# Kernel optimization log

Measured on AMD Instinct MI355X. Metric: run time of the kernel, lower is better.

Reference implementation:

```python
import jax, jax.numpy as jnp
import numpy as np

B, L, D, H = 8, 1024, 512, 8
DH = D // H  # 64
EPS = 1e-5


def setup_inputs() -> dict:
    key = jax.random.key(0)
    ks = jax.random.split(key, 9)
    query = jax.random.normal(ks[0], (B, L, D), dtype=jnp.float32)
    key_t = jax.random.normal(ks[1], (B, L, D), dtype=jnp.float32)
    value = jax.random.normal(ks[2], (B, L, D), dtype=jnp.float32)
    attn_mask = jax.random.bernoulli(ks[3], 0.1, (B, L, L))
    softmax_mask = jax.random.bernoulli(ks[4], 0.1, (B, L, L))
    s = 1.0 / np.sqrt(D)
    Wq = jax.random.uniform(ks[5], (D, D), jnp.float32, -s, s)
    Wk = jax.random.uniform(ks[6], (D, D), jnp.float32, -s, s)
    Wv = jax.random.uniform(ks[7], (D, D), jnp.float32, -s, s)
    Wo = jax.random.uniform(ks[8], (D, D), jnp.float32, -s, s)
    return {"query": query, "key": key_t, "value": value,
            "attn_mask": attn_mask, "softmax_mask": softmax_mask,
            "Wq": Wq, "Wk": Wk, "Wv": Wv, "Wo": Wo}


def _split_heads(x):
    # [B, L, D] -> [B, H, L, DH]
    b, l, _ = x.shape
    return x.reshape(b, l, H, DH).transpose(0, 2, 1, 3)


def reference(query, key, value, attn_mask, softmax_mask, Wq, Wk, Wv, Wo):
    residual = query
    q = _split_heads(query @ Wq.T)   # [B,H,L,DH]
    k = _split_heads(key @ Wk.T)
    v = _split_heads(value @ Wv.T)
    scale = DH ** (-0.5)
    scores = jnp.einsum("bhqd,bhkd->bhqk", q, k) * scale
    scores = jnp.where(attn_mask[:, None], -jnp.inf, scores)
    attention = jax.nn.softmax(scores, axis=-1)
    attention = jnp.where(softmax_mask[:, None], 0.0, attention)
    # dropout p = 0.0 -> identity
    context = jnp.einsum("bhqk,bhkd->bhqd", attention, v)
    context = context.transpose(0, 2, 1, 3).reshape(query.shape[0], -1, D)
    output = context @ Wo.T
    x = residual + output
    mean = jnp.mean(x, axis=-1, keepdims=True)
    var = jnp.var(x, axis=-1, keepdims=True)
    out = (x - mean) * jax.lax.rsqrt(var + EPS)  # LayerNorm, no affine
    return out, attention
```

## Files before the change

### kernel.cpp

```cpp
#include <hip/hip_runtime.h>

#define BB 8
#define LL 1024
#define DD 512
#define HH 8

typedef __attribute__((ext_vector_type(8))) short bf16x8;
typedef __attribute__((ext_vector_type(4))) float f32x4;

__device__ __forceinline__ unsigned short f2bf(float f) {
    union { float f; unsigned u; } c; c.f = f;
    unsigned u = c.u + 0x7fffu + ((c.u >> 16) & 1u);
    return (unsigned short)(u >> 16);
}

__global__ __launch_bounds__(256) void castw_kernel(
    const float* wq, const float* wk, const float* wv, const float* wo,
    unsigned short* wqb, unsigned short* wkb, unsigned short* wvb, unsigned short* wob)
{
    const float* src; unsigned short* dst;
    switch (blockIdx.y) {
        case 0:  src = wq; dst = wqb; break;
        case 1:  src = wk; dst = wkb; break;
        case 2:  src = wv; dst = wvb; break;
        default: src = wo; dst = wob; break;
    }
    const int g = (blockIdx.x * 256 + threadIdx.x) * 8;
    const float4 a = *reinterpret_cast<const float4*>(src + g);
    const float4 b = *reinterpret_cast<const float4*>(src + g + 4);
    uint4 o;
    o.x = (unsigned)f2bf(a.x) | ((unsigned)f2bf(a.y) << 16);
    o.y = (unsigned)f2bf(a.z) | ((unsigned)f2bf(a.w) << 16);
    o.z = (unsigned)f2bf(b.x) | ((unsigned)f2bf(b.y) << 16);
    o.w = (unsigned)f2bf(b.z) | ((unsigned)f2bf(b.w) << 16);
    *reinterpret_cast<uint4*>(dst + g) = o;
}

__global__ __launch_bounds__(256) void maskpack_kernel(
    const int* __restrict__ am, const int* __restrict__ sm,
    unsigned* __restrict__ ab, unsigned* __restrict__ sb)
{
    const int* src = blockIdx.y ? sm : am;
    unsigned* dst  = blockIdx.y ? sb : ab;
    const int l = threadIdx.x & 63;
    for (int g = blockIdx.x * 256 + threadIdx.x; g < 8388608; g += gridDim.x * 256) {
        unsigned long long bm = __ballot(src[g] != 0);
        if (l == 0)  dst[g >> 5] = (unsigned)bm;
        if (l == 32) dst[g >> 5] = (unsigned)(bm >> 32);
    }
}

template<bool OUTBF, bool AF32>
__device__ __forceinline__ void gemm_mfma_body(
    const void* __restrict__ Av, const unsigned short* __restrict__ W,
    void* __restrict__ Yv)
{
    __shared__ unsigned short As[128 * 40];
    __shared__ unsigned short Bs[128 * 40];
    const int t = threadIdx.x, w = t >> 6, lane = t & 63;
    const int ln15 = lane & 15, quad = lane >> 4;
    const int wm = w & 1, wn = w >> 1;
    const int m0 = blockIdx.y * 128, n0 = blockIdx.x * 128;
    f32x4 acc[4][4];
    #pragma unroll
    for (int i = 0; i < 4; i++)
        #pragma unroll
        for (int j = 0; j < 4; j++) acc[i][j] = (f32x4){0.f, 0.f, 0.f, 0.f};

    for (int k0 = 0; k0 < 512; k0 += 32) {
        uint4 ga[2], gb[2];
        #pragma unroll
        for (int i = 0; i < 2; i++) {
            const int u = t + i * 256, row = u >> 2, ch = (u & 3) * 8;
            if (AF32) {
                const float* Af = (const float*)Av;
                const float4 fa = *reinterpret_cast<const float4*>(&Af[(size_t)(m0 + row) * 512 + k0 + ch]);
                const float4 fb = *reinterpret_cast<const float4*>(&Af[(size_t)(m0 + row) * 512 + k0 + ch + 4]);
                ga[i].x = (unsigned)f2bf(fa.x) | ((unsigned)f2bf(fa.y) << 16);
                ga[i].y = (unsigned)f2bf(fa.z) | ((unsigned)f2bf(fa.w) << 16);
                ga[i].z = (unsigned)f2bf(fb.x) | ((unsigned)f2bf(fb.y) << 16);
                ga[i].w = (unsigned)f2bf(fb.z) | ((unsigned)f2bf(fb.w) << 16);
            } else {
                ga[i] = *reinterpret_cast<const uint4*>(
                    &((const unsigned short*)Av)[(size_t)(m0 + row) * 512 + k0 + ch]);
            }
            gb[i] = *reinterpret_cast<const uint4*>(&W[(size_t)(n0 + row) * 512 + k0 + ch]);
        }
        if (k0) __syncthreads();
        #pragma unroll
        for (int i = 0; i < 2; i++) {
            const int u = t + i * 256, row = u >> 2, ch = (u & 3) * 8;
            *reinterpret_cast<uint4*>(&As[row * 40 + ch]) = ga[i];
            *reinterpret_cast<uint4*>(&Bs[row * 40 + ch]) = gb[i];
        }
        __syncthreads();
        bf16x8 af[4], bf_[4];
        #pragma unroll
        for (int s = 0; s < 4; s++) {
            af[s]  = *reinterpret_cast<const bf16x8*>(&As[(wm * 64 + s * 16 + ln15) * 40 + quad * 8]);
            bf_[s] = *reinterpret_cast<const bf16x8*>(&Bs[(wn * 64 + s * 16 + ln15) * 40 + quad * 8]);
        }
        #pragma unroll
        for (int sm_ = 0; sm_ < 4; sm_++)
            #pragma unroll
            for (int sn_ = 0; sn_ < 4; sn_++)
                acc[sm_][sn_] = __builtin_amdgcn_mfma_f32_16x16x32_bf16(
                    af[sm_], bf_[sn_], acc[sm_][sn_], 0, 0, 0);
    }
    #pragma unroll
    for (int sm_ = 0; sm_ < 4; sm_++)
        #pragma unroll
        for (int sn_ = 0; sn_ < 4; sn_++)
            #pragma unroll
            for (int r = 0; r < 4; r++) {
                const int row = m0 + wm * 64 + sm_ * 16 + quad * 4 + r;
                const int col = n0 + wn * 64 + sn_ * 16 + ln15;
                if (OUTBF)
                    ((unsigned short*)Yv)[(size_t)row * 512 + col] = f2bf(acc[sm_][sn_][r]);
                else
                    ((float*)Yv)[(size_t)row * 512 + col] = acc[sm_][sn_][r];
            }
}

__global__ __launch_bounds__(256) void gemm3_kernel(
    const float* a0, const float* a1, const float* a2,
    const unsigned short* w0, const unsigned short* w1, const unsigned short* w2,
    unsigned short* y0, unsigned short* y1, unsigned short* y2)
{
    const float* A; const unsigned short* W; unsigned short* Y;
    if (blockIdx.z == 0)      { A = a0; W = w0; Y = y0; }
    else if (blockIdx.z == 1) { A = a1; W = w1; Y = y1; }
    else                      { A = a2; W = w2; Y = y2; }
    gemm_mfma_body<true, true>(A, W, Y);
}

__global__ __launch_bounds__(256) void gemm1_kernel(
    const unsigned short* A, const unsigned short* W, float* Y)
{
    gemm_mfma_body<false, false>(A, W, Y);
}

__global__ __launch_bounds__(256) void vtrans_kernel(
    const unsigned short* __restrict__ Vb, unsigned short* __restrict__ Vt)
{
    __shared__ unsigned short tile[64 * 72];
    const int t = threadIdx.x;
    const int tt = blockIdx.x, h = blockIdx.y, b = blockIdx.z;
    #pragma unroll
    for (int i = 0; i < 2; i++) {
        const int u = t + i * 256, row = u >> 3, ch = (u & 7) * 8;
        *reinterpret_cast<uint4*>(&tile[row * 72 + ch]) =
            *reinterpret_cast<const uint4*>(&Vb[(size_t)(b * 1024 + tt * 64 + row) * 512 + h * 64 + ch]);
    }
    __syncthreads();
    #pragma unroll
    for (int i = 0; i < 2; i++) {
        const int u = t + i * 256, dh = u >> 3, ch = (u & 7) * 8;
        unsigned short r8[8];
        #pragma unroll
        for (int e = 0; e < 8; e++) r8[e] = tile[(ch + e) * 72 + dh];
        uint4 o;
        o.x = (unsigned)r8[0] | ((unsigned)r8[1] << 16);
        o.y = (unsigned)r8[2] | ((unsigned)r8[3] << 16);
        o.z = (unsigned)r8[4] | ((unsigned)r8[5] << 16);
        o.w = (unsigned)r8[6] | ((unsigned)r8[7] << 16);
        *reinterpret_cast<uint4*>(&Vt[(size_t)((b * 8 + h) * 64 + dh) * 1024 + tt * 64 + ch]) = o;
    }
}

__global__ __launch_bounds__(256) void fattn_kernel(
    const unsigned short* __restrict__ Qb, const unsigned short* __restrict__ Kb,
    const unsigned short* __restrict__ Vt,
    const unsigned* __restrict__ ab, const unsigned* __restrict__ sb,
    float* __restrict__ attn, unsigned short* __restrict__ CTX)
{
    __shared__ __align__(16) unsigned short Ks[64 * 72];
    __shared__ __align__(16) unsigned short Vs[64 * 72];
    __shared__ __align__(16) unsigned short Pt[4][16 * 72];
    const int t = threadIdx.x, w = t >> 6, lane = t & 63;
    const int ln15 = lane & 15, quad = lane >> 4;
    const int id = blockIdx.x;
    const int b = id & 7, slot = id >> 3;
    const int qt = slot & 15, h = slot >> 4;
    const int bh = b * 8 + h;
    const int qbase = qt * 64 + w * 16;

    const int srow = t >> 2, sch = (t & 3) * 16;
    const size_t kg = ((size_t)(b * 1024 + srow)) * 512 + h * 64 + sch;
    const size_t vg = ((size_t)(bh * 64 + srow)) * 1024 + sch;
    unsigned short* ksw = &Ks[srow * 72 + sch];
    unsigned short* vsw = &Vs[srow * 72 + sch];

    const size_t qoff = ((size_t)(b * 1024) + qbase + ln15) * 512 + h * 64 + quad * 8;
    const bf16x8 aq0 = *reinterpret_cast<const bf16x8*>(Qb + qoff);
    const bf16x8 aq1 = *reinterpret_cast<const bf16x8*>(Qb + qoff + 32);

    int mrow[4];
    #pragma unroll
    for (int r = 0; r < 4; r++)
        mrow[r] = (b * 1024 + qbase + quad * 4 + r) * 32;

    uint4 kr0 = *reinterpret_cast<const uint4*>(Kb + kg);
    uint4 kr1 = *reinterpret_cast<const uint4*>(Kb + kg + 8);
    *reinterpret_cast<uint4*>(ksw)     = kr0;
    *reinterpret_cast<uint4*>(ksw + 8) = kr1;
    __syncthreads();

    float l[4];
    #pragma unroll
    for (int r = 0; r < 4; r++) l[r] = 0.f;

    for (int kt = 0; kt < 16; kt++) {
        if (kt < 15) {
            kr0 = *reinterpret_cast<const uint4*>(Kb + kg + (size_t)(kt + 1) * 32768);
            kr1 = *reinterpret_cast<const uint4*>(Kb + kg + (size_t)(kt + 1) * 32768 + 8);
        }
        f32x4 acc[4];
        #pragma unroll
        for (int sub = 0; sub < 4; sub++) {
            const bf16x8 bk0 = *reinterpret_cast<const bf16x8*>(&Ks[(sub * 16 + ln15) * 72 + quad * 8]);
            const bf16x8 bk1 = *reinterpret_cast<const bf16x8*>(&Ks[(sub * 16 + ln15) * 72 + quad * 8 + 32]);
            f32x4 c = __builtin_amdgcn_mfma_f32_16x16x32_bf16(aq0, bk0, (f32x4){0.f,0.f,0.f,0.f}, 0, 0, 0);
            acc[sub] = __builtin_amdgcn_mfma_f32_16x16x32_bf16(aq1, bk1, c, 0, 0, 0);
        }
        #pragma unroll
        for (int r = 0; r < 4; r++) {
            const unsigned w0 = ab[mrow[r] + kt * 2], w1 = ab[mrow[r] + kt * 2 + 1];
            #pragma unroll
            for (int sub = 0; sub < 4; sub++) {
                const int cb = sub * 16 + ln15;
                const unsigned msk = ((cb & 32 ? w1 : w0) >> (cb & 31)) & 1u;
                const float e = __expf(acc[sub][r] * 0.125f);
                l[r] += msk ? 0.f : e;
            }
        }
        __syncthreads();
        if (kt < 15) {
            *reinterpret_cast<uint4*>(ksw)     = kr0;
            *reinterpret_cast<uint4*>(ksw + 8) = kr1;
        }
        __syncthreads();
    }
    float invl[4];
    #pragma unroll
    for (int r = 0; r < 4; r++) {
        #pragma unroll
        for (int off = 1; off < 16; off <<= 1) l[r] += __shfl_xor(l[r], off);
        invl[r] = 1.f / l[r];
    }

    kr0 = *reinterpret_cast<const uint4*>(Kb + kg);
    kr1 = *reinterpret_cast<const uint4*>(Kb + kg + 8);
    uint4 vr0 = *reinterpret_cast<const uint4*>(Vt + vg);
    uint4 vr1 = *reinterpret_cast<const uint4*>(Vt + vg + 8);
    __syncthreads();
    *reinterpret_cast<uint4*>(ksw)     = kr0;
    *reinterpret_cast<uint4*>(ksw + 8) = kr1;
    *reinterpret_cast<uint4*>(vsw)     = vr0;
    *reinterpret_cast<uint4*>(vsw + 8) = vr1;
    __syncthreads();

    f32x4 o[4];
    #pragma unroll
    for (int sn = 0; sn < 4; sn++) o[sn] = (f32x4){0.f, 0.f, 0.f, 0.f};
    unsigned short* Pw = Pt[w];

    for (int kt = 0; kt < 16; kt++) {
        if (kt < 15) {
            kr0 = *reinterpret_cast<const uint4*>(Kb + kg + (size_t)(kt + 1) * 32768);
            kr1 = *reinterpret_cast<const uint4*>(Kb + kg + (size_t)(kt + 1) * 32768 + 8);
            vr0 = *reinterpret_cast<const uint4*>(Vt + vg + (size_t)(kt + 1) * 64);
            vr1 = *reinterpret_cast<const uint4*>(Vt + vg + (size_t)(kt + 1) * 64 + 8);
        }
        f32x4 acc[4];
        #pragma unroll
        for (int sub = 0; sub < 4; sub++) {
            const bf16x8 bk0 = *reinterpret_cast<const bf16x8*>(&Ks[(sub * 16 + ln15) * 72 + quad * 8]);
            const bf16x8 bk1 = *reinterpret_cast<const bf16x8*>(&Ks[(sub * 16 + ln15) * 72 + quad * 8 + 32]);
            f32x4 c = __builtin_amdgcn_mfma_f32_16x16x32_bf16(aq0, bk0, (f32x4){0.f,0.f,0.f,0.f}, 0, 0, 0);
            acc[sub] = __builtin_amdgcn_mfma_f32_16x16x32_bf16(aq1, bk1, c, 0, 0, 0);
        }
        #pragma unroll
        for (int r = 0; r < 4; r++) {
            const unsigned a0 = ab[mrow[r] + kt * 2], a1 = ab[mrow[r] + kt * 2 + 1];
            const unsigned s0 = sb[mrow[r] + kt * 2], s1 = sb[mrow[r] + kt * 2 + 1];
            #pragma unroll
            for (int sub = 0; sub < 4; sub++) {
                const int cb = sub * 16 + ln15;
                const unsigned amsk = ((cb & 32 ? a1 : a0) >> (cb & 31)) & 1u;
                const unsigned smsk = ((cb & 32 ? s1 : s0) >> (cb & 31)) & 1u;
                float a = __expf(acc[sub][r] * 0.125f) * invl[r];
                a = amsk ? 0.f : a;
                a = smsk ? 0.f : a;
                attn[((size_t)bh * 1024 + qbase + quad * 4 + r) * 1024 + kt * 64 + cb] = a;
                Pw[(quad * 4 + r) * 72 + cb] = f2bf(a);
            }
        }
        const bf16x8 pa0 = *reinterpret_cast<const bf16x8*>(&Pw[ln15 * 72 + quad * 8]);
        const bf16x8 pa1 = *reinterpret_cast<const bf16x8*>(&Pw[ln15 * 72 + 32 + quad * 8]);
        #pragma unroll
        for (int sn = 0; sn < 4; sn++) {
            const bf16x8 vb0 = *reinterpret_cast<const bf16x8*>(&Vs[(sn * 16 + ln15) * 72 + quad * 8]);
            const bf16x8 vb1 = *reinterpret_cast<const bf16x8*>(&Vs[(sn * 16 + ln15) * 72 + quad * 8 + 32]);
            o[sn] = __builtin_amdgcn_mfma_f32_16x16x32_bf16(pa0, vb0, o[sn], 0, 0, 0);
            o[sn] = __builtin_amdgcn_mfma_f32_16x16x32_bf16(pa1, vb1, o[sn], 0, 0, 0);
        }
        __syncthreads();
        if (kt < 15) {
            *reinterpret_cast<uint4*>(ksw)     = kr0;
            *reinterpret_cast<uint4*>(ksw + 8) = kr1;
            *reinterpret_cast<uint4*>(vsw)     = vr0;
            *reinterpret_cast<uint4*>(vsw + 8) = vr1;
        }
        __syncthreads();
    }
    #pragma unroll
    for (int sn = 0; sn < 4; sn++)
        #pragma unroll
        for (int r = 0; r < 4; r++)
            CTX[((size_t)(b * 1024) + qbase + quad * 4 + r) * 512 + h * 64 + sn * 16 + ln15] =
                f2bf(o[sn][r]);
}

__global__ __launch_bounds__(256) void ln_kernel(
    const float* __restrict__ X, const float* __restrict__ R,
    float* __restrict__ out)
{
    __shared__ float rs[4], rq[4];
    const int r = blockIdx.x, t = threadIdx.x;
    const float2 xv = *reinterpret_cast<const float2*>(&X[(size_t)r * 512 + 2 * t]);
    const float2 rv = *reinterpret_cast<const float2*>(&R[(size_t)r * 512 + 2 * t]);
    const float x0 = xv.x + rv.x, x1 = xv.y + rv.y;
    float s = x0 + x1, q = x0 * x0 + x1 * x1;
    #pragma unroll
    for (int off = 32; off > 0; off >>= 1) { s += __shfl_xor(s, off); q += __shfl_xor(q, off); }
    if ((t & 63) == 0) { rs[t >> 6] = s; rq[t >> 6] = q; }
    __syncthreads();
    s = rs[0] + rs[1] + rs[2] + rs[3];
    q = rq[0] + rq[1] + rq[2] + rq[3];
    const float mean = s * (1.f / 512.f);
    const float var  = q * (1.f / 512.f) - mean * mean;
    const float rstd = rsqrtf(var + 1e-5f);
    float2 o;
    o.x = (x0 - mean) * rstd;
    o.y = (x1 - mean) * rstd;
    *reinterpret_cast<float2*>(&out[(size_t)r * 512 + 2 * t]) = o;
}

extern "C" void kernel_launch(void* const* d_in, const int* in_sizes, int n_in,
                              void* d_out, int out_size, void* d_ws, size_t ws_size,
                              hipStream_t stream)
{
    const float* q  = (const float*)d_in[0];
    const float* k  = (const float*)d_in[1];
    const float* v  = (const float*)d_in[2];
    const int*   am = (const int*)d_in[3];
    const int*   sm = (const int*)d_in[4];
    const float* wq = (const float*)d_in[5];
    const float* wk = (const float*)d_in[6];
    const float* wv = (const float*)d_in[7];
    const float* wo = (const float*)d_in[8];

    float* out  = (float*)d_out;
    float* attn = out + (size_t)BB * LL * DD;

    unsigned char* W = (unsigned char*)d_ws;
    unsigned short* Vt   = (unsigned short*)(W + 0);
    unsigned short* CTXb = (unsigned short*)(W + 8388608);
    unsigned short* wqbf = (unsigned short*)(W + 25165824);
    unsigned short* wkbf = (unsigned short*)(W + 25690112);
    unsigned short* wvbf = (unsigned short*)(W + 26214400);
    unsigned short* wobf = (unsigned short*)(W + 26738688);
    unsigned*       ab   = (unsigned*)      (W + 27262976);
    unsigned*       sb   = (unsigned*)      (W + 28311552);
    unsigned short* Qbf  = (unsigned short*)(W + 29360128);
    unsigned short* Kbf  = (unsigned short*)(W + 37748736);
    unsigned short* Vbf  = (unsigned short*)(W + 46137344);
    float*          X2f  = (float*)(W + 29360128);

    castw_kernel<<<dim3(128, 4, 1), 256, 0, stream>>>(wq, wk, wv, wo,
        wqbf, wkbf, wvbf, wobf);
    maskpack_kernel<<<dim3(2048, 2, 1), 256, 0, stream>>>(am, sm, ab, sb);
    gemm3_kernel<<<dim3(4, 64, 3), 256, 0, stream>>>(q, k, v,
        wqbf, wkbf, wvbf, Qbf, Kbf, Vbf);
    vtrans_kernel<<<dim3(16, 8, 8), 256, 0, stream>>>(Vbf, Vt);
    fattn_kernel<<<dim3(1024, 1, 1), 256, 0, stream>>>(Qbf, Kbf, Vt, ab, sb, attn, CTXb);
    gemm1_kernel<<<dim3(4, 64, 1), 256, 0, stream>>>(CTXb, wobf, X2f);
    ln_kernel<<<dim3(8192, 1, 1), 256, 0, stream>>>(X2f, q, out);
}
```

Baseline: 525.2 us.

## Double-buffer attention K/V tiles, widen attention blocks, fuse weight cast into GEMMs

The attention kernel now uses 512-thread blocks covering 128 query rows, with K/V shared-memory tiles double-buffered so each key tile needs one barrier instead of two. The separate weight-cast kernel is removed and fp32 weights are converted to bf16 inside the GEMM loads, saving a launch but repeating the conversion in every block. The mask packing kernel reads int4 vectors and combines nibbles with shuffles instead of doing a per-element ballot. Together these target launch overhead, barrier stalls and mask-read efficiency, at the cost of more shared memory per attention block and redundant weight conversions.

```diff
diff --git a/kernel.cpp b/kernel.cpp
--- a/kernel.cpp
+++ b/kernel.cpp
@@ -14,45 +14,44 @@
     return (unsigned short)(u >> 16);
 }
 
-__global__ __launch_bounds__(256) void castw_kernel(
-    const float* wq, const float* wk, const float* wv, const float* wo,
-    unsigned short* wqb, unsigned short* wkb, unsigned short* wvb, unsigned short* wob)
-{
-    const float* src; unsigned short* dst;
-    switch (blockIdx.y) {
-        case 0:  src = wq; dst = wqb; break;
-        case 1:  src = wk; dst = wkb; break;
-        case 2:  src = wv; dst = wvb; break;
-        default: src = wo; dst = wob; break;
-    }
-    const int g = (blockIdx.x * 256 + threadIdx.x) * 8;
-    const float4 a = *reinterpret_cast<const float4*>(src + g);
-    const float4 b = *reinterpret_cast<const float4*>(src + g + 4);
-    uint4 o;
-    o.x = (unsigned)f2bf(a.x) | ((unsigned)f2bf(a.y) << 16);
-    o.y = (unsigned)f2bf(a.z) | ((unsigned)f2bf(a.w) << 16);
-    o.z = (unsigned)f2bf(b.x) | ((unsigned)f2bf(b.y) << 16);
-    o.w = (unsigned)f2bf(b.z) | ((unsigned)f2bf(b.w) << 16);
-    *reinterpret_cast<uint4*>(dst + g) = o;
+template<bool F32SRC>
+__device__ __forceinline__ uint4 ld8bf(const void* base, size_t idx) {
+    if (F32SRC) {
+        const float* p = (const float*)base + idx;
+        const float4 a = *reinterpret_cast<const float4*>(p);
+        const float4 b = *reinterpret_cast<const float4*>(p + 4);
+        uint4 o;
+        o.x = (unsigned)f2bf(a.x) | ((unsigned)f2bf(a.y) << 16);
+        o.y = (unsigned)f2bf(a.z) | ((unsigned)f2bf(a.w) << 16);
+        o.z = (unsigned)f2bf(b.x) | ((unsigned)f2bf(b.y) << 16);
+        o.w = (unsigned)f2bf(b.z) | ((unsigned)f2bf(b.w) << 16);
+        return o;
+    } else {
+        return *reinterpret_cast<const uint4*>((const unsigned short*)base + idx);
+    }
 }
 
 __global__ __launch_bounds__(256) void maskpack_kernel(
     const int* __restrict__ am, const int* __restrict__ sm,
     unsigned* __restrict__ ab, unsigned* __restrict__ sb)
 {
-    const int* src = blockIdx.y ? sm : am;
-    unsigned* dst  = blockIdx.y ? sb : ab;
-    const int l = threadIdx.x & 63;
-    for (int g = blockIdx.x * 256 + threadIdx.x; g < 8388608; g += gridDim.x * 256) {
-        unsigned long long bm = __ballot(src[g] != 0);
-        if (l == 0)  dst[g >> 5] = (unsigned)bm;
-        if (l == 32) dst[g >> 5] = (unsigned)(bm >> 32);
-    }
-}
-
-template<bool OUTBF, bool AF32>
+    const int4* src = reinterpret_cast<const int4*>(blockIdx.y ? sm : am);
+    unsigned* dst   = blockIdx.y ? sb : ab;
+    for (int g = blockIdx.x * 256 + threadIdx.x; g < 2097152; g += gridDim.x * 256) {
+        const int4 x = src[g];
+        unsigned nib = (unsigned)(x.x != 0) | ((unsigned)(x.y != 0) << 1)
+                     | ((unsigned)(x.z != 0) << 2) | ((unsigned)(x.w != 0) << 3);
+        unsigned word = nib << ((g & 7) * 4);
+        word |= __shfl_xor(word, 1);
+        word |= __shfl_xor(word, 2);
+        word |= __shfl_xor(word, 4);
+        if ((threadIdx.x & 7) == 0) dst[g >> 3] = word;
+    }
+}
+
+template<bool OUTBF, bool AF32, bool WF32>
 __device__ __forceinline__ void gemm_mfma_body(
-    const void* __restrict__ Av, const unsigned short* __restrict__ W,
+    const void* __restrict__ Av, const void* __restrict__ Wv,
     void* __restrict__ Yv)
 {
     __shared__ unsigned short As[128 * 40];
@@ -72,19 +71,8 @@
         #pragma unroll
         for (int i = 0; i < 2; i++) {
             const int u = t + i * 256, row = u >> 2, ch = (u & 3) * 8;
-            if (AF32) {
-                const float* Af = (const float*)Av;
-                const float4 fa = *reinterpret_cast<const float4*>(&Af[(size_t)(m0 + row) * 512 + k0 + ch]);
-                const float4 fb = *reinterpret_cast<const float4*>(&Af[(size_t)(m0 + row) * 512 + k0 + ch + 4]);
-                ga[i].x = (unsigned)f2bf(fa.x) | ((unsigned)f2bf(fa.y) << 16);
-                ga[i].y = (unsigned)f2bf(fa.z) | ((unsigned)f2bf(fa.w) << 16);
-                ga[i].z = (unsigned)f2bf(fb.x) | ((unsigned)f2bf(fb.y) << 16);
-                ga[i].w = (unsigned)f2bf(fb.z) | ((unsigned)f2bf(fb.w) << 16);
-            } else {
-                ga[i] = *reinterpret_cast<const uint4*>(
-                    &((const unsigned short*)Av)[(size_t)(m0 + row) * 512 + k0 + ch]);
-            }
-            gb[i] = *reinterpret_cast<const uint4*>(&W[(size_t)(n0 + row) * 512 + k0 + ch]);
+            ga[i] = ld8bf<AF32>(Av, (size_t)(m0 + row) * 512 + k0 + ch);
+            gb[i] = ld8bf<WF32>(Wv, (size_t)(n0 + row) * 512 + k0 + ch);
         }
         if (k0) __syncthreads();
         #pragma unroll
@@ -124,20 +112,20 @@
 
 __global__ __launch_bounds__(256) void gemm3_kernel(
     const float* a0, const float* a1, const float* a2,
-    const unsigned short* w0, const unsigned short* w1, const unsigned short* w2,
+    const float* w0, const float* w1, const float* w2,
     unsigned short* y0, unsigned short* y1, unsigned short* y2)
 {
-    const float* A; const unsigned short* W; unsigned short* Y;
+    const float *A, *W; unsigned short* Y;
     if (blockIdx.z == 0)      { A = a0; W = w0; Y = y0; }
     else if (blockIdx.z == 1) { A = a1; W = w1; Y = y1; }
     else                      { A = a2; W = w2; Y = y2; }
-    gemm_mfma_body<true, true>(A, W, Y);
+    gemm_mfma_body<true, true, true>(A, W, Y);
 }
 
 __global__ __launch_bounds__(256) void gemm1_kernel(
-    const unsigned short* A, const unsigned short* W, float* Y)
-{
-    gemm_mfma_body<false, false>(A, W, Y);
+    const unsigned short* A, const float* W, float* Y)
+{
+    gemm_mfma_body<false, false, true>(A, W, Y);
 }
 
 __global__ __launch_bounds__(256) void vtrans_kernel(
@@ -168,28 +156,27 @@
     }
 }
 
-__global__ __launch_bounds__(256) void fattn_kernel(
+__global__ __launch_bounds__(512) void fattn_kernel(
     const unsigned short* __restrict__ Qb, const unsigned short* __restrict__ Kb,
     const unsigned short* __restrict__ Vt,
     const unsigned* __restrict__ ab, const unsigned* __restrict__ sb,
     float* __restrict__ attn, unsigned short* __restrict__ CTX)
 {
-    __shared__ __align__(16) unsigned short Ks[64 * 72];
-    __shared__ __align__(16) unsigned short Vs[64 * 72];
-    __shared__ __align__(16) unsigned short Pt[4][16 * 72];
+    __shared__ __align__(16) unsigned short Ks[2][64 * 72];
+    __shared__ __align__(16) unsigned short Vs[2][64 * 72];
+    __shared__ __align__(16) unsigned short Pt[8][16 * 72];
     const int t = threadIdx.x, w = t >> 6, lane = t & 63;
     const int ln15 = lane & 15, quad = lane >> 4;
     const int id = blockIdx.x;
     const int b = id & 7, slot = id >> 3;
-    const int qt = slot & 15, h = slot >> 4;
+    const int qt = slot & 7, h = slot >> 3;
     const int bh = b * 8 + h;
-    const int qbase = qt * 64 + w * 16;
-
-    const int srow = t >> 2, sch = (t & 3) * 16;
+    const int qbase = qt * 128 + w * 16;
+
+    const int srow = t >> 3, sch = (t & 7) * 8;
     const size_t kg = ((size_t)(b * 1024 + srow)) * 512 + h * 64 + sch;
     const size_t vg = ((size_t)(bh * 64 + srow)) * 1024 + sch;
-    unsigned short* ksw = &Ks[srow * 72 + sch];
-    unsigned short* vsw = &Vs[srow * 72 + sch];
+    const int sidx = srow * 72 + sch;
 
     const size_t qoff = ((size_t)(b * 1024) + qbase + ln15) * 512 + h * 64 + quad * 8;
     const bf16x8 aq0 = *reinterpret_cast<const bf16x8*>(Qb + qoff);
@@ -200,26 +187,23 @@
     for (int r = 0; r < 4; r++)
         mrow[r] = (b * 1024 + qbase + quad * 4 + r) * 32;
 
-    uint4 kr0 = *reinterpret_cast<const uint4*>(Kb + kg);
-    uint4 kr1 = *reinterpret_cast<const uint4*>(Kb + kg + 8);
-    *reinterpret_cast<uint4*>(ksw)     = kr0;
-    *reinterpret_cast<uint4*>(ksw + 8) = kr1;
+    uint4 kr = *reinterpret_cast<const uint4*>(Kb + kg);
+    *reinterpret_cast<uint4*>(&Ks[0][sidx]) = kr;
     __syncthreads();
 
     float l[4];
     #pragma unroll
     for (int r = 0; r < 4; r++) l[r] = 0.f;
 
+    int cur = 0;
     for (int kt = 0; kt < 16; kt++) {
-        if (kt < 15) {
-            kr0 = *reinterpret_cast<const uint4*>(Kb + kg + (size_t)(kt + 1) * 32768);
-            kr1 = *reinterpret_cast<const uint4*>(Kb + kg + (size_t)(kt + 1) * 32768 + 8);
-        }
+        if (kt < 15)
+            kr = *reinterpret_cast<const uint4*>(Kb + kg + (size_t)(kt + 1) * 32768);
         f32x4 acc[4];
         #pragma unroll
         for (int sub = 0; sub < 4; sub++) {
-            const bf16x8 bk0 = *reinterpret_cast<const bf16x8*>(&Ks[(sub * 16 + ln15) * 72 + quad * 8]);
-            const bf16x8 bk1 = *reinterpret_cast<const bf16x8*>(&Ks[(sub * 16 + ln15) * 72 + quad * 8 + 32]);
+            const bf16x8 bk0 = *reinterpret_cast<const bf16x8*>(&Ks[cur][(sub * 16 + ln15) * 72 + quad * 8]);
+            const bf16x8 bk1 = *reinterpret_cast<const bf16x8*>(&Ks[cur][(sub * 16 + ln15) * 72 + quad * 8 + 32]);
             f32x4 c = __builtin_amdgcn_mfma_f32_16x16x32_bf16(aq0, bk0, (f32x4){0.f,0.f,0.f,0.f}, 0, 0, 0);
             acc[sub] = __builtin_amdgcn_mfma_f32_16x16x32_bf16(aq1, bk1, c, 0, 0, 0);
         }
@@ -234,13 +218,14 @@
                 l[r] += msk ? 0.f : e;
             }
         }
+        if (kt < 15)
+            *reinterpret_cast<uint4*>(&Ks[cur ^ 1][sidx]) = kr;
         __syncthreads();
-        if (kt < 15) {
-            *reinterpret_cast<uint4*>(ksw)     = kr0;
-            *reinterpret_cast<uint4*>(ksw + 8) = kr1;
-        }
-        __syncthreads();
-    }
+        cur ^= 1;
+    }
+
+    kr = *reinterpret_cast<const uint4*>(Kb + kg);
+    uint4 vr = *reinterpret_cast<const uint4*>(Vt + vg);
     float invl[4];
     #pragma unroll
     for (int r = 0; r < 4; r++) {
@@ -248,35 +233,31 @@
         for (int off = 1; off < 16; off <<= 1) l[r] += __shfl_xor(l[r], off);
         invl[r] = 1.f / l[r];
     }
-
-    kr0 = *reinterpret_cast<const uint4*>(Kb + kg);
-    kr1 = *reinterpret_cast<const uint4*>(Kb + kg + 8);
-    uint4 vr0 = *reinterpret_cast<const uint4*>(Vt + vg);
-    uint4 vr1 = *reinterpret_cast<const uint4*>(Vt + vg + 8);
+    *reinterpret_cast<uint4*>(&Ks[0][sidx]) = kr;
+    *reinterpret_cast<uint4*>(&Vs[0][sidx]) = vr;
     __syncthreads();
-    *reinterpret_cast<uint4*>(ksw)     = kr0;
-    *reinterpret_cast<uint4*>(ksw + 8) = kr1;
-    *reinterpret_cast<uint4*>(vsw)     = vr0;
-    *reinterpret_cast<uint4*>(vsw + 8) = vr1;
-    __syncthreads();
+
+    float* ap[4];
+    #pragma unroll
+    for (int r = 0; r < 4; r++)
+        ap[r] = attn + ((size_t)bh * 1024 + qbase + quad * 4 + r) * 1024 + ln15;
 
     f32x4 o[4];
     #pragma unroll
     for (int sn = 0; sn < 4; sn++) o[sn] = (f32x4){0.f, 0.f, 0.f, 0.f};
     unsigned short* Pw = Pt[w];
 
+    cur = 0;
     for (int kt = 0; kt < 16; kt++) {
         if (kt < 15) {
-            kr0 = *reinterpret_cast<const uint4*>(Kb + kg + (size_t)(kt + 1) * 32768);
-            kr1 = *reinterpret_cast<const uint4*>(Kb + kg + (size_t)(kt + 1) * 32768 + 8);
-            vr0 = *reinterpret_cast<const uint4*>(Vt + vg + (size_t)(kt + 1) * 64);
-            vr1 = *reinterpret_cast<const uint4*>(Vt + vg + (size_t)(kt + 1) * 64 + 8);
+            kr = *reinterpret_cast<const uint4*>(Kb + kg + (size_t)(kt + 1) * 32768);
+            vr = *reinterpret_cast<const uint4*>(Vt + vg + (size_t)(kt + 1) * 64);
         }
         f32x4 acc[4];
         #pragma unroll
         for (int sub = 0; sub < 4; sub++) {
-            const bf16x8 bk0 = *reinterpret_cast<const bf16x8*>(&Ks[(sub * 16 + ln15) * 72 + quad * 8]);
-            const bf16x8 bk1 = *reinterpret_cast<const bf16x8*>(&Ks[(sub * 16 + ln15) * 72 + quad * 8 + 32]);
+            const bf16x8 bk0 = *reinterpret_cast<const bf16x8*>(&Ks[cur][(sub * 16 + ln15) * 72 + quad * 8]);
+            const bf16x8 bk1 = *reinterpret_cast<const bf16x8*>(&Ks[cur][(sub * 16 + ln15) * 72 + quad * 8 + 32]);
             f32x4 c = __builtin_amdgcn_mfma_f32_16x16x32_bf16(aq0, bk0, (f32x4){0.f,0.f,0.f,0.f}, 0, 0, 0);
             acc[sub] = __builtin_amdgcn_mfma_f32_16x16x32_bf16(aq1, bk1, c, 0, 0, 0);
         }
@@ -292,7 +273,7 @@
                 float a = __expf(acc[sub][r] * 0.125f) * invl[r];
                 a = amsk ? 0.f : a;
                 a = smsk ? 0.f : a;
-                attn[((size_t)bh * 1024 + qbase + quad * 4 + r) * 1024 + kt * 64 + cb] = a;
+                ap[r][kt * 64 + sub * 16] = a;
                 Pw[(quad * 4 + r) * 72 + cb] = f2bf(a);
             }
         }
@@ -300,19 +281,17 @@
         const bf16x8 pa1 = *reinterpret_cast<const bf16x8*>(&Pw[ln15 * 72 + 32 + quad * 8]);
         #pragma unroll
         for (int sn = 0; sn < 4; sn++) {
-            const bf16x8 vb0 = *reinterpret_cast<const bf16x8*>(&Vs[(sn * 16 + ln15) * 72 + quad * 8]);
-            const bf16x8 vb1 = *reinterpret_cast<const bf16x8*>(&Vs[(sn * 16 + ln15) * 72 + quad * 8 + 32]);
+            const bf16x8 vb0 = *reinterpret_cast<const bf16x8*>(&Vs[cur][(sn * 16 + ln15) * 72 + quad * 8]);
+            const bf16x8 vb1 = *reinterpret_cast<const bf16x8*>(&Vs[cur][(sn * 16 + ln15) * 72 + quad * 8 + 32]);
             o[sn] = __builtin_amdgcn_mfma_f32_16x16x32_bf16(pa0, vb0, o[sn], 0, 0, 0);
             o[sn] = __builtin_amdgcn_mfma_f32_16x16x32_bf16(pa1, vb1, o[sn], 0, 0, 0);
         }
+        if (kt < 15) {
+            *reinterpret_cast<uint4*>(&Ks[cur ^ 1][sidx]) = kr;
+            *reinterpret_cast<uint4*>(&Vs[cur ^ 1][sidx]) = vr;
+        }
         __syncthreads();
-        if (kt < 15) {
-            *reinterpret_cast<uint4*>(ksw)     = kr0;
-            *reinterpret_cast<uint4*>(ksw + 8) = kr1;
-            *reinterpret_cast<uint4*>(vsw)     = vr0;
-            *reinterpret_cast<uint4*>(vsw + 8) = vr1;
-        }
-        __syncthreads();
+        cur ^= 1;
     }
     #pragma unroll
     for (int sn = 0; sn < 4; sn++)
@@ -367,10 +346,6 @@
     unsigned char* W = (unsigned char*)d_ws;
     unsigned short* Vt   = (unsigned short*)(W + 0);
     unsigned short* CTXb = (unsigned short*)(W + 8388608);
-    unsigned short* wqbf = (unsigned short*)(W + 25165824);
-    unsigned short* wkbf = (unsigned short*)(W + 25690112);
-    unsigned short* wvbf = (unsigned short*)(W + 26214400);
-    unsigned short* wobf = (unsigned short*)(W + 26738688);
     unsigned*       ab   = (unsigned*)      (W + 27262976);
     unsigned*       sb   = (unsigned*)      (W + 28311552);
     unsigned short* Qbf  = (unsigned short*)(W + 29360128);
@@ -378,13 +353,11 @@
     unsigned short* Vbf  = (unsigned short*)(W + 46137344);
     float*          X2f  = (float*)(W + 29360128);
 
-    castw_kernel<<<dim3(128, 4, 1), 256, 0, stream>>>(wq, wk, wv, wo,
-        wqbf, wkbf, wvbf, wobf);
     maskpack_kernel<<<dim3(2048, 2, 1), 256, 0, stream>>>(am, sm, ab, sb);
     gemm3_kernel<<<dim3(4, 64, 3), 256, 0, stream>>>(q, k, v,
-        wqbf, wkbf, wvbf, Qbf, Kbf, Vbf);
+        wq, wk, wv, Qbf, Kbf, Vbf);
     vtrans_kernel<<<dim3(16, 8, 8), 256, 0, stream>>>(Vbf, Vt);
-    fattn_kernel<<<dim3(1024, 1, 1), 256, 0, stream>>>(Qbf, Kbf, Vt, ab, sb, attn, CTXb);
-    gemm1_kernel<<<dim3(4, 64, 1), 256, 0, stream>>>(CTXb, wobf, X2f);
+    fattn_kernel<<<dim3(512, 1, 1), 512, 0, stream>>>(Qbf, Kbf, Vt, ab, sb, attn, CTXb);
+    gemm1_kernel<<<dim3(4, 64, 1), 256, 0, stream>>>(CTXb, wo, X2f);
     ln_kernel<<<dim3(8192, 1, 1), 256, 0, stream>>>(X2f, q, out);
 }
```

Result: faster. 498.4 us (-5.1%).
